# Kernel optimization log

Hardware: AMD Instinct MI355X
Metric: run time of the kernel (lower is better)

## Reference

```python
import jax, jax.numpy as jnp
import numpy as np

N_NODES = 100000
N_EDGES = 1600000
NODE_DIM = 128
EDGE_DIM = 32
HIDDEN_DIM = 256


def _linear_params(key, fan_in, fan_out):
    kw, kb = jax.random.split(key)
    bound = 1.0 / np.sqrt(fan_in)
    W = jax.random.uniform(kw, (fan_in, fan_out), minval=-bound, maxval=bound, dtype=jnp.float32)
    b = jax.random.uniform(kb, (fan_out,), minval=-bound, maxval=bound, dtype=jnp.float32)
    return W, b


def setup_inputs() -> dict:
    key = jax.random.key(0)
    ks = jax.random.split(key, 8)
    x = jax.random.normal(ks[0], (N_NODES, NODE_DIM), dtype=jnp.float32)
    edge_index = jax.random.randint(ks[1], (2, N_EDGES), 0, N_NODES, dtype=jnp.int64)
    edge_attr = jax.random.normal(ks[2], (N_EDGES, EDGE_DIM), dtype=jnp.float32)
    congestion = jax.random.uniform(ks[3], (N_NODES,), dtype=jnp.float32)
    msg_in = 2 * NODE_DIM + EDGE_DIM + 1
    mW1, mb1 = _linear_params(ks[4], msg_in, HIDDEN_DIM)
    mW2, mb2 = _linear_params(ks[5], HIDDEN_DIM, NODE_DIM)
    uW1, ub1 = _linear_params(ks[6], 2 * NODE_DIM, HIDDEN_DIM)
    uW2, ub2 = _linear_params(ks[7], HIDDEN_DIM, NODE_DIM)
    return {
        "x": x, "edge_index": edge_index, "edge_attr": edge_attr, "congestion": congestion,
        "mW1": mW1, "mb1": mb1, "mW2": mW2, "mb2": mb2,
        "uW1": uW1, "ub1": ub1, "uW2": uW2, "ub2": ub2,
    }


def reference(x, edge_index, edge_attr, congestion, mW1, mb1, mW2, mb2, uW1, ub1, uW2, ub2):
    src, dst = edge_index[0], edge_index[1]
    # gather node features and src congestion, concat along feature dim  [E, 2D+edge_dim+1]
    msg_in = jnp.concatenate(
        [x[src], x[dst], edge_attr, congestion[src][:, None]], axis=-1)
    h = jax.nn.relu(msg_in @ mW1 + mb1)          # [E, hidden]
    messages = h @ mW2 + mb2                     # [E, node_dim]
    # scatter_add messages into destination nodes  [N, node_dim]
    aggregated = jax.ops.segment_sum(messages, dst, num_segments=x.shape[0])
    upd_in = jnp.concatenate([x, aggregated], axis=-1)  # [N, 2*node_dim]
    h2 = jax.nn.relu(upd_in @ uW1 + ub1)
    x_new = h2 @ uW2 + ub2                       # [N, node_dim]
    return x_new
```

## Files before the change

kernel.cpp:

```cpp
#include <hip/hip_runtime.h>

#define E_TOTAL 1600000
#define NN 100000
#define D 128
#define ED 32
#define H 256

typedef __attribute__((ext_vector_type(8))) short s16x8;
typedef __attribute__((ext_vector_type(4))) short s16x4;
typedef __attribute__((ext_vector_type(4))) float f32x4;

#define MFMA(a, b, c) __builtin_amdgcn_mfma_f32_16x16x32_bf16((a), (b), (c), 0, 0, 0)

__device__ __forceinline__ short f2bf(float f) {
    unsigned u = __builtin_bit_cast(unsigned, f);
    u += 0x7fffu + ((u >> 16) & 1u);
    return (short)(u >> 16);
}
__device__ __forceinline__ float bf2f(short s) {
    return __builtin_bit_cast(float, ((unsigned)(unsigned short)s) << 16);
}

__device__ __forceinline__ void gll16(const void* g, void* l) {
    __builtin_amdgcn_global_load_lds(
        (const __attribute__((address_space(1))) void*)g,
        (__attribute__((address_space(3))) void*)l, 16, 0, 0);
}

__device__ __forceinline__ void swz_one(const float* __restrict__ W,
                                        short* __restrict__ out,
                                        int K, int N, int idx) {
    int j    = idx & 7;
    int lane = (idx >> 3) & 63;
    int rest = idx >> 9;
    int NT   = N >> 4;
    int nt   = rest % NT;
    int t    = rest / NT;
    int k    = t * 32 + (lane >> 4) * 8 + j;
    int col  = nt * 16 + (lane & 15);
    out[idx] = f2bf((k < K) ? W[k * N + col] : 0.f);
}

__device__ __forceinline__ void swz_kp(const float* __restrict__ W,
                                       short* __restrict__ out, int N, int idx) {
    int j    = idx & 7;
    int lane = (idx >> 3) & 63;
    int rest = idx >> 9;
    int NT   = N >> 4;
    int nt   = rest % NT;
    int t    = rest / NT;
    int p    = t * 32 + (lane >> 4) * 8 + j;
    int k    = (p >> 6) * 64 + (p & 3) * 16 + ((p >> 2) & 15);
    int col  = nt * 16 + (lane & 15);
    out[idx] = f2bf(W[k * N + col]);
}

__global__ void k_prep(const float* __restrict__ x, short* __restrict__ xb,
                       const int* __restrict__ ei, int* __restrict__ cnt,
                       const float* __restrict__ mW1, short* __restrict__ W1s,
                       const float* __restrict__ mW2, short* __restrict__ W2s,
                       const float* __restrict__ uW1, short* __restrict__ U1s,
                       const float* __restrict__ uW2, short* __restrict__ U2s) {
    const int b = blockIdx.x;
    if (b < 12500) {
        int i = (b * 256 + threadIdx.x) * 4;
        if (i >= NN * D) return;
        f32x4 v = *(const f32x4*)(x + i);
        s16x4 o;
        o[0] = f2bf(v[0]); o[1] = f2bf(v[1]); o[2] = f2bf(v[2]); o[3] = f2bf(v[3]);
        *(s16x4*)(xb + i) = o;
    } else if (b < 18750) {
        int e = (b - 12500) * 256 + threadIdx.x;
        if (e < E_TOTAL) atomicAdd(&cnt[ei[E_TOTAL + e]], 1);
    } else {
        int idx = (b - 18750) * 256 + threadIdx.x;
        if (idx < 81920) { swz_one(mW1, W1s, 289, 256, idx); return; }
        idx -= 81920;
        if (idx < 32768) { swz_kp(mW2, W2s, 128, idx); return; }
        idx -= 32768;
        if (idx < 65536) { swz_one(uW1, U1s, 256, 256, idx); return; }
        idx -= 65536;
        if (idx < 32768) { swz_kp(uW2, U2s, 128, idx); }
    }
}

__global__ void k_scanc(int* __restrict__ cnt, unsigned long long* __restrict__ chain,
                        const float* __restrict__ b2, float* __restrict__ agg,
                        int n) {
    __shared__ int wsum[16];
    __shared__ int woff[16];
    __shared__ int carry_s;
    __shared__ int deg_s[1024];
    const int tid = threadIdx.x, lane = tid & 63, wv = tid >> 6;
    int i = blockIdx.x * 1024 + tid;
    int v = (i < n) ? cnt[i] : 0;
    int s = v;
#pragma unroll
    for (int off = 1; off < 64; off <<= 1) {
        int u = __shfl_up(s, off, 64);
        if (lane >= off) s += u;
    }
    if (lane == 63) wsum[wv] = s;
    __syncthreads();
    if (wv == 0 && lane < 16) {
        int t = wsum[lane];
        int sc = t;
#pragma unroll
        for (int off = 1; off < 16; off <<= 1) {
            int u = __shfl_up(sc, off, 16);
            if (lane >= off) sc += u;
        }
        woff[lane] = sc - t;
    }
    __syncthreads();
    int excl = (s - v) + woff[wv];
    if (tid == 1023) {
        int btot = excl + v;
        __hip_atomic_store(&chain[blockIdx.x], (1ull << 32) | (unsigned)btot,
                           __ATOMIC_RELAXED, __HIP_MEMORY_SCOPE_AGENT);
        int pfx = 0;
        for (int j = (int)blockIdx.x - 1; j >= 0; --j) {
            unsigned long long e;
            do {
                e = __hip_atomic_load(&chain[j], __ATOMIC_RELAXED,
                                      __HIP_MEMORY_SCOPE_AGENT);
            } while ((e >> 32) == 0);
            pfx += (int)(unsigned)e;
            if ((e >> 32) == 2) break;
        }
        __hip_atomic_store(&chain[blockIdx.x], (2ull << 32) | (unsigned)(pfx + btot),
                           __ATOMIC_RELAXED, __HIP_MEMORY_SCOPE_AGENT);
        carry_s = pfx;
    }
    deg_s[tid] = v;
    __syncthreads();
    if (i < n) cnt[i] = excl + carry_s;

    const int base = blockIdx.x * 1024;
#pragma unroll
    for (int it = 0; it < 32; it++) {
        int idx  = it * 1024 + tid;
        int node = base + (idx >> 5);
        if (node < n) {
            float deg = (float)deg_s[idx >> 5];
            int c = (idx & 31) * 4;
            f32x4 bv = *(const f32x4*)(b2 + c);
            f32x4 o;
#pragma unroll
            for (int j = 0; j < 4; j++) o[j] = deg * bv[j];
            *(f32x4*)(agg + (long)node * D + c) = o;
        }
    }
}

__global__ void k_perm(const int* __restrict__ ei, int* __restrict__ cursor,
                       int* __restrict__ perm, int2* __restrict__ srcdst) {
    int e = blockIdx.x * blockDim.x + threadIdx.x;
    if (e >= E_TOTAL) return;
    int s = ei[e], d = ei[E_TOTAL + e];
    int pos = atomicAdd(&cursor[d], 1);
    perm[pos] = e;
    srcdst[pos] = make_int2(s, d);
}

__global__ __launch_bounds__(512, 4)
void k_pre(const short* __restrict__ xb, const short* __restrict__ W1s,
           const float* __restrict__ b1, short* __restrict__ ys,
           short* __restrict__ yd) {
    __shared__ char smem[32768];
    const int tid  = threadIdx.x;
    const int lane = tid & 63;
    const int w    = tid >> 6;
    const int eh   = w >> 2;
    const int cg   = w & 3;
    const int m    = lane & 15;
    const int q    = lane >> 4;
    const int r0   = blockIdx.x * 128;

    {
        int rowl = w * 16 + (lane >> 2);
        int grow = r0 + rowl;
        int gc   = grow < NN ? grow : 0;
        int kqs  = (lane & 3) ^ ((lane >> 3) & 3);
        const char* gx = (const char*)xb + (long)gc * 256 + kqs * 16;
#pragma unroll
        for (int t = 0; t < 4; t++)
            gll16(gx + t * 64, smem + t * 8192 + w * 1024);
    }
    __syncthreads();

    const int rdoff = m * 64 + ((q ^ ((m >> 1) & 3)) << 4);

    float b1c[4];
#pragma unroll
    for (int n = 0; n < 4; n++) b1c[n] = b1[cg * 64 + n * 16 + m];

#pragma unroll
    for (int pass = 0; pass < 2; pass++) {
        f32x4 acc[4][4];
#pragma unroll
        for (int mt = 0; mt < 4; mt++)
#pragma unroll
            for (int n = 0; n < 4; n++) acc[mt][n] = (f32x4){0.f, 0.f, 0.f, 0.f};
#pragma unroll
        for (int t = 0; t < 4; t++) {
            s16x8 b[4];
            const short* bw = W1s + ((pass * 4 + t) * 16 + cg * 4) * 512 + lane * 8;
#pragma unroll
            for (int n = 0; n < 4; n++) b[n] = *(const s16x8*)(bw + n * 512);
#pragma unroll
            for (int mt = 0; mt < 4; mt++) {
                s16x8 a = *(const s16x8*)(smem + t * 8192 + (eh * 4 + mt) * 1024 + rdoff);
#pragma unroll
                for (int n = 0; n < 4; n++) acc[mt][n] = MFMA(a, b[n], acc[mt][n]);
            }
        }
        short* out = pass ? yd : ys;
#pragma unroll
        for (int mt = 0; mt < 4; mt++)
#pragma unroll
            for (int r = 0; r < 4; r++) {
                int grow = r0 + eh * 64 + mt * 16 + q * 4 + r;
                if (grow < NN) {
                    s16x4 o;
#pragma unroll
                    for (int n = 0; n < 4; n++)
                        o[n] = f2bf(acc[mt][n][r] + (pass ? 0.f : b1c[n]));
                    *(s16x4*)(out + (long)grow * 256 + (cg * 16 + m) * 4) = o;
                }
            }
    }
}

__global__ __launch_bounds__(512, 4)
void k_edge(const int* __restrict__ perm, const int2* __restrict__ srcdst,
            const short* __restrict__ ys, const short* __restrict__ yd,
            const float* __restrict__ eattr, const float* __restrict__ cong,
            const short* __restrict__ W1s, const short* __restrict__ W2s,
            float* __restrict__ agg) {
    __shared__ char smem[73728];
    __shared__ int   dst_s[128];
    __shared__ int   src_s[128];
    __shared__ short cong_s[128];

    const int tid  = threadIdx.x;
    const int lane = tid & 63;
    const int w    = tid >> 6;
    const int eh   = w >> 2;
    const int cg   = w & 3;
    const int m    = lane & 15;
    const int q    = lane >> 4;
    const int p0b  = blockIdx.x * 128;

    {
        int edge = w * 16 + (lane >> 2);
        int kqs  = (lane & 3) ^ ((lane >> 3) & 3);
        int ea = perm[p0b + edge];
        const float* ge = eattr + (long)ea * ED + kqs * 8;
        f32x4 e0 = *(const f32x4*)ge, e1 = *(const f32x4*)(ge + 4);
        s16x8 ev;
#pragma unroll
        for (int j = 0; j < 4; j++) { ev[j] = f2bf(e0[j]); ev[4 + j] = f2bf(e1[j]); }
        *(s16x8*)(smem + w * 1024 + lane * 16) = ev;
        if (tid < 128) {
            int2 sd2 = srcdst[p0b + tid];
            dst_s[tid]  = sd2.y;
            src_s[tid]  = sd2.x;
            cong_s[tid] = f2bf(cong[sd2.x]);
        }
    }
    __syncthreads();

    const int rdoff = m * 64 + ((q ^ ((m >> 1) & 3)) << 4);

    f32x4 acc[4][4];
#pragma unroll
    for (int mt = 0; mt < 4; mt++)
#pragma unroll
        for (int n = 0; n < 4; n++) acc[mt][n] = (f32x4){0.f, 0.f, 0.f, 0.f};

    {
        s16x8 b[4];
        const short* bw = W1s + (8 * 16 + cg * 4) * 512 + lane * 8;
#pragma unroll
        for (int n = 0; n < 4; n++) b[n] = *(const s16x8*)(bw + n * 512);
#pragma unroll
        for (int mt = 0; mt < 4; mt++) {
            s16x8 a = *(const s16x8*)(smem + (eh * 4 + mt) * 1024 + rdoff);
#pragma unroll
            for (int n = 0; n < 4; n++) acc[mt][n] = MFMA(a, b[n], acc[mt][n]);
        }
    }
    {
        s16x8 b[4];
        const short* bw = W1s + (9 * 16 + cg * 4) * 512 + lane * 8;
#pragma unroll
        for (int n = 0; n < 4; n++) b[n] = *(const s16x8*)(bw + n * 512);
#pragma unroll
        for (int mt = 0; mt < 4; mt++) {
            s16x8 a = (s16x8){0, 0, 0, 0, 0, 0, 0, 0};
            short cv = cong_s[eh * 64 + mt * 16 + m];
            a[0] = (q == 0) ? cv : (short)0;
#pragma unroll
            for (int n = 0; n < 4; n++) acc[mt][n] = MFMA(a, b[n], acc[mt][n]);
        }
    }

    {
        char* hbase = smem + 8192;
        const int qoff = (cg * 16 + m) * 4;
        const int s0   = (cg * 16 + m) >> 1;
        const int half = (m & 1) * 8;
#pragma unroll
        for (int mt = 0; mt < 4; mt++) {
            s16x4 ysv[4], ydv[4];
#pragma unroll
            for (int r = 0; r < 4; r++) {
                int e = eh * 64 + mt * 16 + q * 4 + r;
                ysv[r] = *(const s16x4*)(ys + (long)src_s[e] * 256 + qoff);
                ydv[r] = *(const s16x4*)(yd + (long)dst_s[e] * 256 + qoff);
            }
#pragma unroll
            for (int r = 0; r < 4; r++) {
                int e = eh * 64 + mt * 16 + q * 4 + r;
                int sl = s0 ^ (e & 31);
                s16x4 o;
#pragma unroll
                for (int n = 0; n < 4; n++) {
                    float v = acc[mt][n][r] + bf2f(ysv[r][n]) + bf2f(ydv[r][n]);
                    o[n] = f2bf(v > 0.f ? v : 0.f);
                }
                *(s16x4*)(hbase + e * 512 + sl * 16 + half) = o;
            }
        }
    }
    __syncthreads();

    f32x4 acc2[4][2];
#pragma unroll
    for (int mt = 0; mt < 4; mt++) {
        acc2[mt][0] = (f32x4){0.f, 0.f, 0.f, 0.f};
        acc2[mt][1] = (f32x4){0.f, 0.f, 0.f, 0.f};
    }
#pragma unroll
    for (int t2 = 0; t2 < 8; t2++) {
        const short* bw = W2s + (t2 * 8 + cg * 2) * 512 + lane * 8;
        s16x8 b0  = *(const s16x8*)bw;
        s16x8 b1v = *(const s16x8*)(bw + 512);
#pragma unroll
        for (int mt = 0; mt < 4; mt++) {
            int e  = eh * 64 + mt * 16 + m;
            int sl = (t2 * 4 + q) ^ (e & 31);
            s16x8 a = *(const s16x8*)(smem + 8192 + e * 512 + sl * 16);
            acc2[mt][0] = MFMA(a, b0, acc2[mt][0]);
            acc2[mt][1] = MFMA(a, b1v, acc2[mt][1]);
        }
    }
    __syncthreads();

    {
        float (*mbuf)[132] = (float (*)[132])smem;
#pragma unroll
        for (int mt = 0; mt < 4; mt++)
#pragma unroll
            for (int r = 0; r < 4; r++) {
                int edge = eh * 64 + mt * 16 + q * 4 + r;
                mbuf[edge][cg * 32 + m]      = acc2[mt][0][r];
                mbuf[edge][cg * 32 + 16 + m] = acc2[mt][1][r];
            }
    }
    __syncthreads();

    {
        float (*mbuf)[132] = (float (*)[132])smem;
        const int qtr = tid >> 7, cc = tid & 127;
        float s = 0.f;
        int prev = dst_s[qtr * 32];
        for (int row = qtr * 32; row < qtr * 32 + 32; row++) {
            int dcur = dst_s[row];
            if (dcur != prev) {
                __hip_atomic_fetch_add(agg + (long)prev * D + cc, s,
                                       __ATOMIC_RELAXED, __HIP_MEMORY_SCOPE_AGENT);
                s = 0.f; prev = dcur;
            }
            s += mbuf[row][cc];
        }
        __hip_atomic_fetch_add(agg + (long)prev * D + cc, s,
                               __ATOMIC_RELAXED, __HIP_MEMORY_SCOPE_AGENT);
    }
}

__global__ __launch_bounds__(512, 4)
void k_node(const short* __restrict__ xb, const float* __restrict__ agg,
            const short* __restrict__ U1s, const float* __restrict__ b1,
            const short* __restrict__ U2s, const float* __restrict__ b2,
            float* __restrict__ out) {
    __shared__ char smem[65536];
    const int tid  = threadIdx.x;
    const int lane = tid & 63;
    const int w    = tid >> 6;
    const int eh   = w >> 2;
    const int cg   = w & 3;
    const int m    = lane & 15;
    const int q    = lane >> 4;
    const int r0   = blockIdx.x * 128;

    {
        int rowl = w * 16 + (lane >> 2);
        int grow = r0 + rowl;
        int gc   = grow < NN ? grow : 0;
        int kqs  = (lane & 3) ^ ((lane >> 3) & 3);
        const char* gx = (const char*)xb + (long)gc * 256 + kqs * 16;
#pragma unroll
        for (int t = 0; t < 4; t++)
            gll16(gx + t * 64, smem + t * 8192 + w * 1024);
        const float* ga = agg + (long)gc * D + kqs * 8;
#pragma unroll
        for (int t = 0; t < 4; t++) {
            f32x4 a0 = *(const f32x4*)(ga + t * 32);
            f32x4 a1 = *(const f32x4*)(ga + t * 32 + 4);
            s16x8 v;
#pragma unroll
            for (int j = 0; j < 4; j++) { v[j] = f2bf(a0[j]); v[4 + j] = f2bf(a1[j]); }
            *(s16x8*)(smem + (4 + t) * 8192 + w * 1024 + lane * 16) = v;
        }
    }
    __syncthreads();

    const int rdoff = m * 64 + ((q ^ ((m >> 1) & 3)) << 4);

    f32x4 acc[4][4];
#pragma unroll
    for (int mt = 0; mt < 4; mt++)
#pragma unroll
        for (int n = 0; n < 4; n++) acc[mt][n] = (f32x4){0.f, 0.f, 0.f, 0.f};

#pragma unroll
    for (int t = 0; t < 8; t++) {
        s16x8 b[4];
        const short* bw = U1s + (t * 16 + cg * 4) * 512 + lane * 8;
#pragma unroll
        for (int n = 0; n < 4; n++) b[n] = *(const s16x8*)(bw + n * 512);
#pragma unroll
        for (int mt = 0; mt < 4; mt++) {
            s16x8 a = *(const s16x8*)(smem + t * 8192 + (eh * 4 + mt) * 1024 + rdoff);
#pragma unroll
            for (int n = 0; n < 4; n++) acc[mt][n] = MFMA(a, b[n], acc[mt][n]);
        }
    }
    __syncthreads();

    {
        char* hbase = smem;
        const int s0   = (cg * 16 + m) >> 1;
        const int half = (m & 1) * 8;
        float b1c[4];
#pragma unroll
        for (int n = 0; n < 4; n++) b1c[n] = b1[cg * 64 + n * 16 + m];
#pragma unroll
        for (int mt = 0; mt < 4; mt++) {
#pragma unroll
            for (int r = 0; r < 4; r++) {
                int row = eh * 64 + mt * 16 + q * 4 + r;
                int sl  = s0 ^ (row & 31);
                s16x4 o;
#pragma unroll
                for (int n = 0; n < 4; n++) {
                    float v = acc[mt][n][r] + b1c[n];
                    o[n] = f2bf(v > 0.f ? v : 0.f);
                }
                *(s16x4*)(hbase + row * 512 + sl * 16 + half) = o;
            }
        }
    }
    __syncthreads();

    f32x4 acc2[4][2];
#pragma unroll
    for (int mt = 0; mt < 4; mt++) {
        acc2[mt][0] = (f32x4){0.f, 0.f, 0.f, 0.f};
        acc2[mt][1] = (f32x4){0.f, 0.f, 0.f, 0.f};
    }
#pragma unroll
    for (int t2 = 0; t2 < 8; t2++) {
        const short* bw = U2s + (t2 * 8 + cg * 2) * 512 + lane * 8;
        s16x8 b0  = *(const s16x8*)bw;
        s16x8 b1v = *(const s16x8*)(bw + 512);
#pragma unroll
        for (int mt = 0; mt < 4; mt++) {
            int row = eh * 64 + mt * 16 + m;
            int sl  = (t2 * 4 + q) ^ (row & 31);
            s16x8 a = *(const s16x8*)(smem + row * 512 + sl * 16);
            acc2[mt][0] = MFMA(a, b0, acc2[mt][0]);
            acc2[mt][1] = MFMA(a, b1v, acc2[mt][1]);
        }
    }

    {
        float bb0 = b2[cg * 32 + m];
        float bb1 = b2[cg * 32 + 16 + m];
#pragma unroll
        for (int mt = 0; mt < 4; mt++)
#pragma unroll
            for (int r = 0; r < 4; r++) {
                int grow = r0 + eh * 64 + mt * 16 + q * 4 + r;
                if (grow < NN) {
                    out[(long)grow * D + cg * 32 + m]      = acc2[mt][0][r] + bb0;
                    out[(long)grow * D + cg * 32 + 16 + m] = acc2[mt][1][r] + bb1;
                }
            }
    }
}

extern "C" void kernel_launch(void* const* d_in, const int* in_sizes, int n_in,
                              void* d_out, int out_size, void* d_ws, size_t ws_size,
                              hipStream_t stream) {
    const float* x     = (const float*)d_in[0];
    const int*   ei    = (const int*)d_in[1];
    const float* eattr = (const float*)d_in[2];
    const float* cong  = (const float*)d_in[3];
    const float* mW1   = (const float*)d_in[4];
    const float* mb1   = (const float*)d_in[5];
    const float* mW2   = (const float*)d_in[6];
    const float* mb2   = (const float*)d_in[7];
    const float* uW1   = (const float*)d_in[8];
    const float* ub1   = (const float*)d_in[9];
    const float* uW2   = (const float*)d_in[10];
    const float* ub2   = (const float*)d_in[11];

    char* ws = (char*)d_ws;
    float* agg    = (float*)ws;
    short* xb     = (short*)(ws + 51200000);
    short* W1s    = (short*)(ws + 76800000);
    short* W2s    = (short*)(ws + 76963840);
    short* U1s    = (short*)(ws + 77029376);
    short* U2s    = (short*)(ws + 77160448);
    int*   cnt    = (int*)(ws + 77225984);
    unsigned long long* chain = (unsigned long long*)(ws + 77625984);
    int*   perm   = (int*)(ws + 77627008);
    int2*  srcdst = (int2*)(ws + 84027008);
    short* yd     = (short*)(ws + 96827008);
    short* ys     = (short*)(ws + 148027008);

    hipMemsetAsync(cnt, 0, 401024, stream);

    k_prep<<<19582, 256, 0, stream>>>(x, xb, ei, cnt,
                                      mW1, W1s, mW2, W2s, uW1, U1s, uW2, U2s);

    k_pre<<<(NN + 127) / 128, 512, 0, stream>>>(xb, W1s, mb1, ys, yd);

    int nb = (NN + 1023) / 1024;
    k_scanc<<<nb, 1024, 0, stream>>>(cnt, chain, mb2, agg, NN);

    k_perm<<<(E_TOTAL + 255) / 256, 256, 0, stream>>>(ei, cnt, perm, srcdst);

    k_edge<<<E_TOTAL / 128, 512, 0, stream>>>(perm, srcdst, ys, yd, eattr, cong,
                                              W1s, W2s, agg);
    k_node<<<(NN + 127) / 128, 512, 0, stream>>>(xb, agg, U1s, ub1, U2s, ub2,
                                                 (float*)d_out);
}
```

Before: 932.2 us.

## Fold congestion term into per-node precompute, split agg init, use packed bf16 convert

The congestion contribution (cong[src] times the last row of mW1) moves out of the per-edge kernel into the per-node source projection in k_pre. This removes one MFMA k-tile per edge tile and the per-edge gather of cong. The agg bias initialisation moves out of the serial-chained scan kernel into a separate fully parallel kernel that derives degree from the prefix sums. Manual bf16 rounding is replaced with the hardware v_cvt_pk_bf16_f32 instruction throughout. Congestion now goes through bf16 as part of the summed ys value rather than separately, which slightly changes rounding, and the extra launch adds a little overhead.

Result: faster. 904.9 us (-2.9%).

```diff
diff --git a/kernel.cpp b/kernel.cpp
--- a/kernel.cpp
+++ b/kernel.cpp
@@ -20,6 +20,13 @@
 __device__ __forceinline__ float bf2f(short s) {
     return __builtin_bit_cast(float, ((unsigned)(unsigned short)s) << 16);
 }
+__device__ __forceinline__ unsigned cvtpk(float a, float b) {
+    unsigned r;
+    asm("v_cvt_pk_bf16_f32 %0, %1, %2" : "=v"(r) : "v"(a), "v"(b));
+    return r;
+}
+union u_s16x4 { s16x4 v; unsigned u[2]; };
+union u_s16x8 { s16x8 v; unsigned u[4]; };
 
 __device__ __forceinline__ void gll16(const void* g, void* l) {
     __builtin_amdgcn_global_load_lds(
@@ -66,9 +73,10 @@
         int i = (b * 256 + threadIdx.x) * 4;
         if (i >= NN * D) return;
         f32x4 v = *(const f32x4*)(x + i);
-        s16x4 o;
-        o[0] = f2bf(v[0]); o[1] = f2bf(v[1]); o[2] = f2bf(v[2]); o[3] = f2bf(v[3]);
-        *(s16x4*)(xb + i) = o;
+        u_s16x4 o;
+        o.u[0] = cvtpk(v[0], v[1]);
+        o.u[1] = cvtpk(v[2], v[3]);
+        *(s16x4*)(xb + i) = o.v;
     } else if (b < 18750) {
         int e = (b - 12500) * 256 + threadIdx.x;
         if (e < E_TOTAL) atomicAdd(&cnt[ei[E_TOTAL + e]], 1);
@@ -85,12 +93,10 @@
 }
 
 __global__ void k_scanc(int* __restrict__ cnt, unsigned long long* __restrict__ chain,
-                        const float* __restrict__ b2, float* __restrict__ agg,
                         int n) {
     __shared__ int wsum[16];
     __shared__ int woff[16];
     __shared__ int carry_s;
-    __shared__ int deg_s[1024];
     const int tid = threadIdx.x, lane = tid & 63, wv = tid >> 6;
     int i = blockIdx.x * 1024 + tid;
     int v = (i < n) ? cnt[i] : 0;
@@ -132,25 +138,24 @@
                            __ATOMIC_RELAXED, __HIP_MEMORY_SCOPE_AGENT);
         carry_s = pfx;
     }
-    deg_s[tid] = v;
     __syncthreads();
     if (i < n) cnt[i] = excl + carry_s;
-
-    const int base = blockIdx.x * 1024;
-#pragma unroll
-    for (int it = 0; it < 32; it++) {
-        int idx  = it * 1024 + tid;
-        int node = base + (idx >> 5);
-        if (node < n) {
-            float deg = (float)deg_s[idx >> 5];
-            int c = (idx & 31) * 4;
-            f32x4 bv = *(const f32x4*)(b2 + c);
-            f32x4 o;
-#pragma unroll
-            for (int j = 0; j < 4; j++) o[j] = deg * bv[j];
-            *(f32x4*)(agg + (long)node * D + c) = o;
-        }
-    }
+}
+
+__global__ void k_agginit(const int* __restrict__ cnt, const float* __restrict__ b2,
+                          float* __restrict__ agg) {
+    int i4 = (blockIdx.x * 256 + threadIdx.x) * 4;
+    if (i4 >= NN * D) return;
+    int node  = i4 >> 7;
+    int c     = i4 & 127;
+    int start = cnt[node];
+    int end   = (node < NN - 1) ? cnt[node + 1] : E_TOTAL;
+    float deg = (float)(end - start);
+    f32x4 bv = *(const f32x4*)(b2 + c);
+    f32x4 o;
+#pragma unroll
+    for (int j = 0; j < 4; j++) o[j] = deg * bv[j];
+    *(f32x4*)(agg + i4) = o;
 }
 
 __global__ void k_perm(const int* __restrict__ ei, int* __restrict__ cursor,
@@ -165,7 +170,8 @@
 
 __global__ __launch_bounds__(512, 4)
 void k_pre(const short* __restrict__ xb, const short* __restrict__ W1s,
-           const float* __restrict__ b1, short* __restrict__ ys,
+           const float* __restrict__ b1, const float* __restrict__ cong,
+           const float* __restrict__ w288, short* __restrict__ ys,
            short* __restrict__ yd) {
     __shared__ char smem[32768];
     const int tid  = threadIdx.x;
@@ -191,9 +197,12 @@
 
     const int rdoff = m * 64 + ((q ^ ((m >> 1) & 3)) << 4);
 
-    float b1c[4];
-#pragma unroll
-    for (int n = 0; n < 4; n++) b1c[n] = b1[cg * 64 + n * 16 + m];
+    float b1c[4], w288c[4];
+#pragma unroll
+    for (int n = 0; n < 4; n++) {
+        b1c[n]   = b1[cg * 64 + n * 16 + m];
+        w288c[n] = w288[cg * 64 + n * 16 + m];
+    }
 
 #pragma unroll
     for (int pass = 0; pass < 2; pass++) {
@@ -222,11 +231,20 @@
             for (int r = 0; r < 4; r++) {
                 int grow = r0 + eh * 64 + mt * 16 + q * 4 + r;
                 if (grow < NN) {
-                    s16x4 o;
-#pragma unroll
-                    for (int n = 0; n < 4; n++)
-                        o[n] = f2bf(acc[mt][n][r] + (pass ? 0.f : b1c[n]));
-                    *(s16x4*)(out + (long)grow * 256 + (cg * 16 + m) * 4) = o;
+                    float vv[4];
+                    if (pass == 0) {
+                        float cv = cong[grow];
+#pragma unroll
+                        for (int n = 0; n < 4; n++)
+                            vv[n] = acc[mt][n][r] + b1c[n] + cv * w288c[n];
+                    } else {
+#pragma unroll
+                        for (int n = 0; n < 4; n++) vv[n] = acc[mt][n][r];
+                    }
+                    u_s16x4 o;
+                    o.u[0] = cvtpk(vv[0], vv[1]);
+                    o.u[1] = cvtpk(vv[2], vv[3]);
+                    *(s16x4*)(out + (long)grow * 256 + (cg * 16 + m) * 4) = o.v;
                 }
             }
     }
@@ -235,13 +253,12 @@
 __global__ __launch_bounds__(512, 4)
 void k_edge(const int* __restrict__ perm, const int2* __restrict__ srcdst,
             const short* __restrict__ ys, const short* __restrict__ yd,
-            const float* __restrict__ eattr, const float* __restrict__ cong,
+            const float* __restrict__ eattr,
             const short* __restrict__ W1s, const short* __restrict__ W2s,
             float* __restrict__ agg) {
     __shared__ char smem[73728];
-    __shared__ int   dst_s[128];
-    __shared__ int   src_s[128];
-    __shared__ short cong_s[128];
+    __shared__ int dst_s[128];
+    __shared__ int src_s[128];
 
     const int tid  = threadIdx.x;
     const int lane = tid & 63;
@@ -258,15 +275,16 @@
         int ea = perm[p0b + edge];
         const float* ge = eattr + (long)ea * ED + kqs * 8;
         f32x4 e0 = *(const f32x4*)ge, e1 = *(const f32x4*)(ge + 4);
-        s16x8 ev;
-#pragma unroll
-        for (int j = 0; j < 4; j++) { ev[j] = f2bf(e0[j]); ev[4 + j] = f2bf(e1[j]); }
-        *(s16x8*)(smem + w * 1024 + lane * 16) = ev;
+        u_s16x8 ev;
+        ev.u[0] = cvtpk(e0[0], e0[1]);
+        ev.u[1] = cvtpk(e0[2], e0[3]);
+        ev.u[2] = cvtpk(e1[0], e1[1]);
+        ev.u[3] = cvtpk(e1[2], e1[3]);
+        *(s16x8*)(smem + w * 1024 + lane * 16) = ev.v;
         if (tid < 128) {
             int2 sd2 = srcdst[p0b + tid];
-            dst_s[tid]  = sd2.y;
-            src_s[tid]  = sd2.x;
-            cong_s[tid] = f2bf(cong[sd2.x]);
+            dst_s[tid] = sd2.y;
+            src_s[tid] = sd2.x;
         }
     }
     __syncthreads();
@@ -278,7 +296,6 @@
     for (int mt = 0; mt < 4; mt++)
 #pragma unroll
         for (int n = 0; n < 4; n++) acc[mt][n] = (f32x4){0.f, 0.f, 0.f, 0.f};
-
     {
         s16x8 b[4];
         const short* bw = W1s + (8 * 16 + cg * 4) * 512 + lane * 8;
@@ -287,20 +304,6 @@
 #pragma unroll
         for (int mt = 0; mt < 4; mt++) {
             s16x8 a = *(const s16x8*)(smem + (eh * 4 + mt) * 1024 + rdoff);
-#pragma unroll
-            for (int n = 0; n < 4; n++) acc[mt][n] = MFMA(a, b[n], acc[mt][n]);
-        }
-    }
-    {
-        s16x8 b[4];
-        const short* bw = W1s + (9 * 16 + cg * 4) * 512 + lane * 8;
-#pragma unroll
-        for (int n = 0; n < 4; n++) b[n] = *(const s16x8*)(bw + n * 512);
-#pragma unroll
-        for (int mt = 0; mt < 4; mt++) {
-            s16x8 a = (s16x8){0, 0, 0, 0, 0, 0, 0, 0};
-            short cv = cong_s[eh * 64 + mt * 16 + m];
-            a[0] = (q == 0) ? cv : (short)0;
 #pragma unroll
             for (int n = 0; n < 4; n++) acc[mt][n] = MFMA(a, b[n], acc[mt][n]);
         }
@@ -324,13 +327,16 @@
             for (int r = 0; r < 4; r++) {
                 int e = eh * 64 + mt * 16 + q * 4 + r;
                 int sl = s0 ^ (e & 31);
-                s16x4 o;
+                float vv[4];
 #pragma unroll
                 for (int n = 0; n < 4; n++) {
                     float v = acc[mt][n][r] + bf2f(ysv[r][n]) + bf2f(ydv[r][n]);
-                    o[n] = f2bf(v > 0.f ? v : 0.f);
+                    vv[n] = v > 0.f ? v : 0.f;
                 }
-                *(s16x4*)(hbase + e * 512 + sl * 16 + half) = o;
+                u_s16x4 o;
+                o.u[0] = cvtpk(vv[0], vv[1]);
+                o.u[1] = cvtpk(vv[2], vv[3]);
+                *(s16x4*)(hbase + e * 512 + sl * 16 + half) = o.v;
             }
         }
     }
@@ -419,10 +425,12 @@
         for (int t = 0; t < 4; t++) {
             f32x4 a0 = *(const f32x4*)(ga + t * 32);
             f32x4 a1 = *(const f32x4*)(ga + t * 32 + 4);
-            s16x8 v;
-#pragma unroll
-            for (int j = 0; j < 4; j++) { v[j] = f2bf(a0[j]); v[4 + j] = f2bf(a1[j]); }
-            *(s16x8*)(smem + (4 + t) * 8192 + w * 1024 + lane * 16) = v;
+            u_s16x8 v;
+            v.u[0] = cvtpk(a0[0], a0[1]);
+            v.u[1] = cvtpk(a0[2], a0[3]);
+            v.u[2] = cvtpk(a1[0], a1[1]);
+            v.u[3] = cvtpk(a1[2], a1[3]);
+            *(s16x8*)(smem + (4 + t) * 8192 + w * 1024 + lane * 16) = v.v;
         }
     }
     __syncthreads();
@@ -461,15 +469,18 @@
         for (int mt = 0; mt < 4; mt++) {
 #pragma unroll
             for (int r = 0; r < 4; r++) {
-                int row = eh * 64 + mt * 16 + q * 4 + r;
+                int row = mt * 16 + q * 4 + r + eh * 64;
                 int sl  = s0 ^ (row & 31);
-                s16x4 o;
+                float vv[4];
 #pragma unroll
                 for (int n = 0; n < 4; n++) {
                     float v = acc[mt][n][r] + b1c[n];
-                    o[n] = f2bf(v > 0.f ? v : 0.f);
+                    vv[n] = v > 0.f ? v : 0.f;
                 }
-                *(s16x4*)(hbase + row * 512 + sl * 16 + half) = o;
+                u_s16x4 o;
+                o.u[0] = cvtpk(vv[0], vv[1]);
+                o.u[1] = cvtpk(vv[2], vv[3]);
+                *(s16x4*)(hbase + row * 512 + sl * 16 + half) = o.v;
             }
         }
     }
@@ -547,14 +558,17 @@
     k_prep<<<19582, 256, 0, stream>>>(x, xb, ei, cnt,
                                       mW1, W1s, mW2, W2s, uW1, U1s, uW2, U2s);
 
-    k_pre<<<(NN + 127) / 128, 512, 0, stream>>>(xb, W1s, mb1, ys, yd);
+    k_pre<<<(NN + 127) / 128, 512, 0, stream>>>(xb, W1s, mb1, cong,
+                                                mW1 + 288 * 256, ys, yd);
 
     int nb = (NN + 1023) / 1024;
-    k_scanc<<<nb, 1024, 0, stream>>>(cnt, chain, mb2, agg, NN);
+    k_scanc<<<nb, 1024, 0, stream>>>(cnt, chain, NN);
+
+    k_agginit<<<12500, 256, 0, stream>>>(cnt, mb2, agg);
 
     k_perm<<<(E_TOTAL + 255) / 256, 256, 0, stream>>>(ei, cnt, perm, srcdst);
 
-    k_edge<<<E_TOTAL / 128, 512, 0, stream>>>(perm, srcdst, ys, yd, eattr, cong,
+    k_edge<<<E_TOTAL / 128, 512, 0, stream>>>(perm, srcdst, ys, yd, eattr,
                                               W1s, W2s, agg);
     k_node<<<(NN + 127) / 128, 512, 0, stream>>>(xb, agg, U1s, ub1, U2s, ub2,
                                                  (float*)d_out);
```
